# Performance work log

Hardware: AMD Instinct MI355X
Metric: run time of the kernel (lower is better)

The kernel has to match this reference:

```python
import jax, jax.numpy as jnp
import numpy as np

N_NODES = 10000
N_EDGES = 160000
N_GRAPHS = 64
HID = 128
EDGE_DIM = 1
NODE_DIM = 3
LAT = 64
N_LAYERS = 3


def _ln(x, g, b, eps=1e-5):
    m = jnp.mean(x, axis=-1, keepdims=True)
    v = jnp.mean((x - m) ** 2, axis=-1, keepdims=True)
    return (x - m) * jax.lax.rsqrt(v + eps) * g + b


def _lin(x, W, b):
    # torch nn.Linear convention: W is [out, in]
    return x @ W.T + b


def setup_inputs() -> dict:
    key = jax.random.key(0)
    ks = jax.random.split(key, 24)
    s = 0.05
    inp = {
        "x": jax.random.normal(ks[0], (N_NODES, NODE_DIM), jnp.float32),
        "edge_attr": jax.random.normal(ks[1], (N_EDGES, EDGE_DIM), jnp.float32),
        "edge_index": jax.random.randint(ks[2], (2, N_EDGES), 0, N_NODES, jnp.int32),
        "batch": jnp.sort(jax.random.randint(ks[3], (N_NODES,), 0, N_GRAPHS, jnp.int32)),
        # node embedding
        "emb_W": jax.random.normal(ks[4], (HID, NODE_DIM), jnp.float32) * s,
        "emb_b": jnp.zeros((HID,), jnp.float32),
        "emb_ln_g": jnp.ones((HID,), jnp.float32),
        "emb_ln_b": jnp.zeros((HID,), jnp.float32),
        # conv layers (stacked over L)
        "msg1_W": jax.random.normal(ks[5], (N_LAYERS, 2 * HID, 2 * HID + EDGE_DIM), jnp.float32) * s,
        "msg1_b": jnp.zeros((N_LAYERS, 2 * HID), jnp.float32),
        "msg2_W": jax.random.normal(ks[6], (N_LAYERS, HID, 2 * HID), jnp.float32) * s,
        "msg2_b": jnp.zeros((N_LAYERS, HID), jnp.float32),
        "gate_W": jax.random.normal(ks[7], (N_LAYERS, HID, 2 * HID), jnp.float32) * s,
        "gate_b": jnp.zeros((N_LAYERS, HID), jnp.float32),
        "ln_g": jnp.ones((N_LAYERS, HID), jnp.float32),
        "ln_b": jnp.zeros((N_LAYERS, HID), jnp.float32),
        # projector
        "proj1_W": jax.random.normal(ks[8], (HID, HID), jnp.float32) * s,
        "proj1_b": jnp.zeros((HID,), jnp.float32),
        "proj_ln1_g": jnp.ones((HID,), jnp.float32),
        "proj_ln1_b": jnp.zeros((HID,), jnp.float32),
        "proj2_W": jax.random.normal(ks[9], (LAT, HID), jnp.float32) * s,
        "proj2_b": jnp.zeros((LAT,), jnp.float32),
        "proj_ln2_g": jnp.ones((LAT,), jnp.float32),
        "proj_ln2_b": jnp.zeros((LAT,), jnp.float32),
    }
    return inp


def reference(x, edge_attr, edge_index, batch,
              emb_W, emb_b, emb_ln_g, emb_ln_b,
              msg1_W, msg1_b, msg2_W, msg2_b, gate_W, gate_b, ln_g, ln_b,
              proj1_W, proj1_b, proj_ln1_g, proj_ln1_b,
              proj2_W, proj2_b, proj_ln2_g, proj_ln2_b):
    src, dst = edge_index[0], edge_index[1]  # PyG flow source_to_target: x_j=x[src], x_i=x[dst]
    # node embedding
    h = jax.nn.silu(_ln(_lin(x, emb_W, emb_b), emb_ln_g, emb_ln_b))
    for l in range(N_LAYERS):
        z = jnp.concatenate([h[dst], h[src], edge_attr], axis=-1)  # [E, 2H+ed]
        m = jax.nn.silu(_lin(z, msg1_W[l], msg1_b[l]))             # [E, 2H]
        m = _lin(m, msg2_W[l], msg2_b[l])                          # [E, H]
        aggr = jax.ops.segment_sum(m, dst, num_segments=N_NODES)   # scatter-add
        gate = jax.nn.sigmoid(_lin(jnp.concatenate([h, aggr], axis=-1), gate_W[l], gate_b[l]))
        h_new = gate * aggr + (1.0 - gate) * h
        h = _ln(h + h_new, ln_g[l], ln_b[l])
    # global pooling
    counts = jax.ops.segment_sum(jnp.ones((N_NODES,), h.dtype), batch, num_segments=N_GRAPHS)
    sums = jax.ops.segment_sum(h, batch, num_segments=N_GRAPHS)    # [G, H]
    x_mean = sums / jnp.maximum(counts, 1.0)[:, None]
    x_max = sums / (counts[:, None] + 1e-6)
    x_global = x_mean + x_max
    # projector
    p = jax.nn.silu(_ln(_lin(x_global, proj1_W, proj1_b), proj_ln1_g, proj_ln1_b))
    z_out = _ln(_lin(p, proj2_W, proj2_b), proj_ln2_g, proj_ln2_b)
    return z_out, x_global
```

## Files before the change

kernel.cpp:

```cpp
#include <hip/hip_runtime.h>

#define NN 10000
#define NNP 10048
#define NE 160000
#define NG 64
#define HID 128
#define NL 3
#define CAP 64

typedef float floatx4 __attribute__((ext_vector_type(4)));
typedef _Float16 f16x8 __attribute__((ext_vector_type(8)));
typedef __fp16 f16x2 __attribute__((ext_vector_type(2)));

__device__ __forceinline__ float fsig(float x){
  return __builtin_amdgcn_rcpf(1.f + __expf(-x));
}

#define RZ_A (2*65536)
#define RZ_B (RZ_A + NL*32768)
#define RZ_C (RZ_B + NL*32768)
#define RZ_D (RZ_C + NL*256)
#define RB1  1283
#define RB2  (RB1 + 625)
#define RB3  (RB2 + 628)

__global__ __launch_bounds__(256) void k_setup(
    const float* __restrict__ m1, const float* __restrict__ m2,
    const float* __restrict__ mg, const float* __restrict__ m1b,
    const int* __restrict__ ei, const float* __restrict__ ea,
    const float* __restrict__ x,
    const float* __restrict__ eW, const float* __restrict__ eB,
    const float* __restrict__ eG, const float* __restrict__ eBB,
    _Float16* __restrict__ wnf, _Float16* __restrict__ w2f,
    _Float16* __restrict__ gwf, float* __restrict__ w256,
    int* __restrict__ deg, int* __restrict__ esrc2, float* __restrict__ eas2,
    float* __restrict__ hg, _Float16* __restrict__ hfg, _Float16* __restrict__ UV0)
{
  const int bid = blockIdx.x, tid = threadIdx.x;
  if (bid < RB1){
    int i = bid*256 + tid;
    if (i < RZ_A){
      int l = (i>>16) + 1, j = i & 65535;
      int t=j&7, col=(j>>3)&15, quad=(j>>7)&3, s=(j>>9)&3, mb=(j>>11)&31;
      int o = mb*16+col, k = s*32+quad*8+t;
      float v = (o<256) ? m1[l*65792 + o*257 + k] : m1[l*65792 + (o-256)*257 + 128 + k];
      wnf[i] = (_Float16)v;
    } else if (i < RZ_B){
      int j=i-RZ_A; int l=j>>15; j&=32767;
      int t=j&7, col=(j>>3)&15, quad=(j>>7)&3, s=(j>>9)&7, mb=(j>>12)&7;
      w2f[(l<<15)+j] = (_Float16)m2[l*32768 + (mb*16+col)*256 + s*32+quad*8+t];
    } else if (i < RZ_C){
      int j=i-RZ_B; int l=j>>15; j&=32767;
      int t=j&7, col=(j>>3)&15, quad=(j>>7)&3, s=(j>>9)&7, mb=(j>>12)&7;
      gwf[(l<<15)+j] = (_Float16)mg[l*32768 + (mb*16+col)*256 + s*32+quad*8+t];
    } else if (i < RZ_D){
      int j=i-RZ_C; int l=j>>8, o=j&255;
      w256[j] = m1[l*65792 + o*257 + 256];
    }
    return;
  }
  if (bid < RB2){
    int e = (bid-RB1)*256 + tid;
    int d = ei[NE + e];
    int slot = atomicAdd(&deg[d], 1) & (CAP-1);
    esrc2[d*CAP + slot] = ei[e];
    eas2[d*CAP + slot]  = ea[e];
    return;
  }
  __shared__ _Float16 HFs[16][136];
  const int tb = bid - RB2;
  {
    int n = tid>>4, q = tid&15;
    int node = tb*16 + n;
    float x0=0.f, x1=0.f, x2=0.f;
    if (node < NN){ x0=x[node*3]; x1=x[node*3+1]; x2=x[node*3+2]; }
    float v[8], s=0.f, s2=0.f;
#pragma unroll
    for (int j=0;j<8;j++){
      int c = q*8+j;
      v[j] = eW[c*3]*x0 + eW[c*3+1]*x1 + eW[c*3+2]*x2 + eB[c];
      s += v[j]; s2 += v[j]*v[j];
    }
#pragma unroll
    for (int m=1;m<16;m<<=1){ s += __shfl_xor(s,m,64); s2 += __shfl_xor(s2,m,64); }
    float mean = s*(1.f/128.f);
    float var  = s2*(1.f/128.f) - mean*mean;
    float rsq  = rsqrtf(var + 1e-5f);
    float ho[8];
#pragma unroll
    for (int j=0;j<8;j++){
      int c = q*8+j;
      float y = (v[j]-mean)*rsq*eG[c] + eBB[c];
      ho[j] = y * fsig(y);
    }
    *(float4*)(hg + (size_t)node*HID + q*8)     = make_float4(ho[0],ho[1],ho[2],ho[3]);
    *(float4*)(hg + (size_t)node*HID + q*8 + 4) = make_float4(ho[4],ho[5],ho[6],ho[7]);
    union { f16x2 h2[4]; uint4 u; } pk;
    pk.h2[0] = __builtin_amdgcn_cvt_pkrtz(ho[0],ho[1]);
    pk.h2[1] = __builtin_amdgcn_cvt_pkrtz(ho[2],ho[3]);
    pk.h2[2] = __builtin_amdgcn_cvt_pkrtz(ho[4],ho[5]);
    pk.h2[3] = __builtin_amdgcn_cvt_pkrtz(ho[6],ho[7]);
    *(uint4*)(hfg + (size_t)node*HID + q*8) = pk.u;
    *(uint4*)(&HFs[n][q*8]) = pk.u;
  }
  __syncthreads();
  {
    const int wv=tid>>6, lane=tid&63, col=lane&15, quad=lane>>4;
    const int node = tb*16 + col;
    f16x8 bf[4];
#pragma unroll
    for (int s=0;s<4;s++) bf[s] = *(const f16x8*)(&HFs[col][s*32+quad*8]);
#pragma unroll
    for (int mt=0;mt<8;mt++){
      int row = (wv*8+mt)*16 + col;
      const float* wrow = (row<256) ? (m1 + row*257) : (m1 + (row-256)*257 + 128);
      floatx4 acc = (floatx4)(0.f);
#pragma unroll
      for (int s=0;s<4;s++){
        const float* wp = wrow + s*32 + quad*8;
        union { f16x2 h2[4]; f16x8 v8; } pa;
        pa.h2[0] = __builtin_amdgcn_cvt_pkrtz(wp[0],wp[1]);
        pa.h2[1] = __builtin_amdgcn_cvt_pkrtz(wp[2],wp[3]);
        pa.h2[2] = __builtin_amdgcn_cvt_pkrtz(wp[4],wp[5]);
        pa.h2[3] = __builtin_amdgcn_cvt_pkrtz(wp[6],wp[7]);
        acc = __builtin_amdgcn_mfma_f32_16x16x32_f16(pa.v8, bf[s], acc, 0,0,0);
      }
      int o0 = (wv*8+mt)*16 + quad*4;
      float4 bv = (o0 < 256) ? *(const float4*)(m1b + o0) : make_float4(0.f,0.f,0.f,0.f);
      union { f16x2 h2[2]; uint2 u; } pk;
      pk.h2[0] = __builtin_amdgcn_cvt_pkrtz(acc[0]+bv.x, acc[1]+bv.y);
      pk.h2[1] = __builtin_amdgcn_cvt_pkrtz(acc[2]+bv.z, acc[3]+bv.w);
      *(uint2*)(UV0 + (size_t)node*512 + o0) = pk.u;
    }
  }
}

__global__ __launch_bounds__(512) void k_layer(
    const _Float16* __restrict__ uvin, _Float16* __restrict__ uvout,
    const int* __restrict__ esrc2, const float* __restrict__ eas2,
    const int* __restrict__ deg,
    const float* __restrict__ w256l,
    const _Float16* __restrict__ w2fl, const float* __restrict__ b2l,
    const _Float16* __restrict__ gwfl, const float* __restrict__ gbl,
    const float* __restrict__ lngl, const float* __restrict__ lnbl,
    float* __restrict__ hg, _Float16* __restrict__ hfg,
    const _Float16* __restrict__ wnfN, const float* __restrict__ m1bN)
{
  __shared__ _Float16 AggH[16][264];
  __shared__ float    Agg[16][132];
  __shared__ float    reds[8][16], reds2[8][16];
  const int tid = threadIdx.x;
  const int wv = tid>>6, lane = tid&63;
  const int col = lane&15, quad = lane>>4;
  const int half = lane>>5, sub = lane&31;
  const int n0 = blockIdx.x*16;

  {
    const int el = sub*8;
    float wcv[8];
    { float4 a = *(const float4*)(w256l + el);
      float4 b = *(const float4*)(w256l + el + 4);
      wcv[0]=a.x; wcv[1]=a.y; wcv[2]=a.z; wcv[3]=a.w;
      wcv[4]=b.x; wcv[5]=b.y; wcv[6]=b.z; wcv[7]=b.w; }
#pragma unroll
    for (int i=0;i<2;i++){
      int nl = wv*2 + i;
      int n = n0 + nl;
      f16x8 uvec = *(const f16x8*)(uvin + (size_t)n*512 + el);
      float U[8], a[8];
#pragma unroll
      for (int j=0;j<8;j++){ U[j] = (float)uvec[j]; a[j] = 0.f; }
      int dg = deg[n]; if (dg > CAP) dg = CAP;
      int r = half;
      if (r < dg){
        const int*   sp = esrc2 + n*CAP;
        const float* ep = eas2 + n*CAP;
        int src = sp[r]; float eav = ep[r];
        f16x8 vb = *(const f16x8*)(uvin + (size_t)src*512 + 256 + el);
        for (;;){
          int rn = r + 2;
          f16x8 vcur = vb; float eac = eav;
          if (rn < dg){
            int s2 = sp[rn]; eav = ep[rn];
            vb = *(const f16x8*)(uvin + (size_t)s2*512 + 256 + el);
          }
#pragma unroll
          for (int j=0;j<8;j++){
            float f = U[j] + (float)vcur[j] + eac*wcv[j];
            a[j] += f*fsig(f);
          }
          if (rn >= dg) break;
          r = rn;
        }
      }
#pragma unroll
      for (int j=0;j<8;j++) a[j] += __shfl_xor(a[j], 32, 64);
      if (half == 0){
        union { f16x2 h2[4]; uint4 u; } pk;
        pk.h2[0] = __builtin_amdgcn_cvt_pkrtz(a[0],a[1]);
        pk.h2[1] = __builtin_amdgcn_cvt_pkrtz(a[2],a[3]);
        pk.h2[2] = __builtin_amdgcn_cvt_pkrtz(a[4],a[5]);
        pk.h2[3] = __builtin_amdgcn_cvt_pkrtz(a[6],a[7]);
        *(uint4*)(&AggH[nl][el]) = pk.u;
      }
    }
  }
  __syncthreads();

  floatx4 acc2 = (floatx4)(0.f);
  {
    const _Float16* wb2 = w2fl + quad*128 + col*8;
#pragma unroll
    for (int s=0;s<8;s++){
      f16x8 b = *(const f16x8*)(&AggH[col][s*32 + quad*8]);
      f16x8 a = *(const f16x8*)(wb2 + (size_t)(wv*8+s)*512);
      acc2 = __builtin_amdgcn_mfma_f32_16x16x32_f16(a, b, acc2, 0,0,0);
    }
  }
  __syncthreads();
  {
    float degf = (float)deg[n0+col];
    int outb = wv*16 + quad*4;
    float4 b2v = *(const float4*)(b2l + outb);
    float v0 = acc2[0] + degf*b2v.x;
    float v1 = acc2[1] + degf*b2v.y;
    float v2 = acc2[2] + degf*b2v.z;
    float v3 = acc2[3] + degf*b2v.w;
    *(float4*)(&Agg[col][outb]) = make_float4(v0,v1,v2,v3);
    union { f16x2 h2[2]; uint2 u; } pk;
    pk.h2[0] = __builtin_amdgcn_cvt_pkrtz(v0,v1);
    pk.h2[1] = __builtin_amdgcn_cvt_pkrtz(v2,v3);
    *(uint2*)(&AggH[col][outb]) = pk.u;
  }
  __syncthreads();

  floatx4 accg = (floatx4)(0.f);
  {
    const int node = n0 + col;
    const _Float16* wbg = gwfl + quad*128 + col*8;
#pragma unroll
    for (int s=0;s<4;s++){
      f16x8 b = *(const f16x8*)(hfg + (size_t)node*HID + s*32 + quad*8);
      f16x8 a = *(const f16x8*)(wbg + (size_t)(wv*8+s)*512);
      accg = __builtin_amdgcn_mfma_f32_16x16x32_f16(a, b, accg, 0,0,0);
    }
#pragma unroll
    for (int s=4;s<8;s++){
      f16x8 b = *(const f16x8*)(&AggH[col][(s-4)*32 + quad*8]);
      f16x8 a = *(const f16x8*)(wbg + (size_t)(wv*8+s)*512);
      accg = __builtin_amdgcn_mfma_f32_16x16x32_f16(a, b, accg, 0,0,0);
    }
  }
  const int outb = wv*16 + quad*4;
  const int node = n0 + col;
  float vvv[4], ss=0.f, ss2=0.f;
  {
    float4 gbv = *(const float4*)(gbl + outb);
    float4 av  = *(const float4*)(&Agg[col][outb]);
    float4 hv  = *(const float4*)(hg + (size_t)node*HID + outb);
    float gg[4] = {gbv.x,gbv.y,gbv.z,gbv.w};
    float aa[4] = {av.x,av.y,av.z,av.w};
    float hh[4] = {hv.x,hv.y,hv.z,hv.w};
#pragma unroll
    for (int r=0;r<4;r++){
      float gate = fsig(accg[r] + gg[r]);
      float v = hh[r] + gate*aa[r] + (1.f-gate)*hh[r];
      vvv[r] = v; ss += v; ss2 += v*v;
    }
  }
  ss  += __shfl_xor(ss, 16, 64);  ss  += __shfl_xor(ss, 32, 64);
  ss2 += __shfl_xor(ss2, 16, 64); ss2 += __shfl_xor(ss2, 32, 64);
  if (quad == 0){ reds[wv][col] = ss; reds2[wv][col] = ss2; }
  __syncthreads();

  {
    float S=0.f, S2=0.f;
#pragma unroll
    for (int w=0;w<8;w++){ S += reds[w][col]; S2 += reds2[w][col]; }
    float mean = S*(1.f/128.f);
    float var  = S2*(1.f/128.f) - mean*mean;
    float rsq  = rsqrtf(var + 1e-5f);
    float4 gv = *(const float4*)(lngl + outb);
    float4 bv = *(const float4*)(lnbl + outb);
    float o0 = (vvv[0]-mean)*rsq*gv.x + bv.x;
    float o1 = (vvv[1]-mean)*rsq*gv.y + bv.y;
    float o2 = (vvv[2]-mean)*rsq*gv.z + bv.z;
    float o3 = (vvv[3]-mean)*rsq*gv.w + bv.w;
    *(float4*)(hg + (size_t)node*HID + outb) = make_float4(o0,o1,o2,o3);
    union { f16x2 h2[2]; uint2 u; } pk;
    pk.h2[0] = __builtin_amdgcn_cvt_pkrtz(o0,o1);
    pk.h2[1] = __builtin_amdgcn_cvt_pkrtz(o2,o3);
    *(uint2*)(hfg + (size_t)node*HID + outb) = pk.u;
    *(uint2*)(&AggH[col][128 + outb]) = pk.u;
  }
  __syncthreads();

  if (uvout){
    f16x8 bf[4];
#pragma unroll
    for (int s=0;s<4;s++) bf[s] = *(const f16x8*)(&AggH[col][128 + s*32 + quad*8]);
    floatx4 au[4];
#pragma unroll
    for (int i=0;i<4;i++) au[i] = (floatx4)(0.f);
    const _Float16* wbn = wnfN + quad*128 + col*8;
#pragma unroll
    for (int s=0;s<4;s++)
#pragma unroll
      for (int mt=0;mt<4;mt++){
        f16x8 a = *(const f16x8*)(wbn + (size_t)((wv*4+mt)*4+s)*512);
        au[mt] = __builtin_amdgcn_mfma_f32_16x16x32_f16(a, bf[s], au[mt], 0,0,0);
      }
#pragma unroll
    for (int mt=0;mt<4;mt++){
      int o0i = (wv*4+mt)*16 + quad*4;
      float4 buv = (o0i < 256) ? *(const float4*)(m1bN + o0i) : make_float4(0.f,0.f,0.f,0.f);
      union { f16x2 h2[2]; uint2 u; } pu;
      pu.h2[0] = __builtin_amdgcn_cvt_pkrtz(au[mt][0]+buv.x, au[mt][1]+buv.y);
      pu.h2[1] = __builtin_amdgcn_cvt_pkrtz(au[mt][2]+buv.z, au[mt][3]+buv.w);
      *(uint2*)(uvout + (size_t)node*512 + o0i) = pu.u;
    }
  }
}

__global__ __launch_bounds__(512) void k_fin(
    const float* __restrict__ h, const int* __restrict__ batch,
    const float* __restrict__ p1W, const float* __restrict__ p1b,
    const float* __restrict__ l1g, const float* __restrict__ l1b,
    const float* __restrict__ p2W, const float* __restrict__ p2b,
    const float* __restrict__ l2g, const float* __restrict__ l2b,
    float* __restrict__ out)
{
  __shared__ float xs[4][128];
  __shared__ float xg[128], pbuf[128], redf[4];
  const int g = blockIdx.x, tid = threadIdx.x;
  const int c = tid & 127, part = tid >> 7;
  int lo, hi;
  { int L=0, r=NN;
    while (L<r){ int m=(L+r)>>1; if (batch[m]<g) L=m+1; else r=m; }
    lo = L; r = NN;
    while (L<r){ int m=(L+r)>>1; if (batch[m]<g+1) L=m+1; else r=m; }
    hi = L; }
  float s = 0.f;
  for (int n = lo+part; n < hi; n += 4) s += h[(size_t)n*HID + c];
  xs[part][c] = s;
  __syncthreads();
  if (tid < 128){
    float cnt = (float)(hi-lo);
    float S = xs[0][c]+xs[1][c]+xs[2][c]+xs[3][c];
    float xgv = S * (1.f/fmaxf(cnt,1.f) + 1.f/(cnt + 1e-6f));
    out[NG*64 + g*HID + c] = xgv;
    xg[c] = xgv;
  }
  __syncthreads();
  {
    float vp = 0.f;
    for (int k = part*32; k < (part+1)*32; k++) vp += xg[k]*p1W[c*HID + k];
    xs[part][c] = vp;
  }
  __syncthreads();
  float v = 0.f;
  if (tid < 128){
    v = p1b[c] + xs[0][c]+xs[1][c]+xs[2][c]+xs[3][c];
    float sv=v, sv2=v*v;
#pragma unroll
    for (int m=1;m<64;m<<=1){ sv+=__shfl_xor(sv,m,64); sv2+=__shfl_xor(sv2,m,64); }
    if ((c&63)==0){ redf[(c>>6)*2]=sv; redf[(c>>6)*2+1]=sv2; }
  }
  __syncthreads();
  if (tid < 128){
    float S=redf[0]+redf[2], S2=redf[1]+redf[3];
    float mean=S*(1.f/128.f), var=S2*(1.f/128.f)-mean*mean;
    float y=(v-mean)*rsqrtf(var+1e-5f)*l1g[c]+l1b[c];
    pbuf[c] = y*fsig(y);
  }
  __syncthreads();
  if (tid < 64){
    float z = p2b[tid];
    for (int k=0;k<HID;k++) z += pbuf[k]*p2W[tid*HID + k];
    float t=z, t2=z*z;
#pragma unroll
    for (int m=1;m<64;m<<=1){ t+=__shfl_xor(t,m,64); t2+=__shfl_xor(t2,m,64); }
    float mn=t*(1.f/64.f), vr=t2*(1.f/64.f)-mn*mn;
    out[g*64 + tid] = (z-mn)*rsqrtf(vr+1e-5f)*l2g[tid]+l2b[tid];
  }
}

extern "C" void kernel_launch(void* const* d_in, const int* in_sizes, int n_in,
                              void* d_out, int out_size, void* d_ws, size_t ws_size,
                              hipStream_t stream){
  const float* x     = (const float*)d_in[0];
  const float* ea    = (const float*)d_in[1];
  const int*   ei    = (const int*)  d_in[2];
  const int*   batch = (const int*)  d_in[3];
  const float* embW  = (const float*)d_in[4];
  const float* embB  = (const float*)d_in[5];
  const float* embG  = (const float*)d_in[6];
  const float* embBe = (const float*)d_in[7];
  const float* m1W   = (const float*)d_in[8];
  const float* m1b   = (const float*)d_in[9];
  const float* m2W   = (const float*)d_in[10];
  const float* m2b   = (const float*)d_in[11];
  const float* gW    = (const float*)d_in[12];
  const float* gb    = (const float*)d_in[13];
  const float* lng   = (const float*)d_in[14];
  const float* lnb   = (const float*)d_in[15];
  const float* p1W   = (const float*)d_in[16];
  const float* p1b   = (const float*)d_in[17];
  const float* l1g   = (const float*)d_in[18];
  const float* l1b   = (const float*)d_in[19];
  const float* p2W   = (const float*)d_in[20];
  const float* p2b   = (const float*)d_in[21];
  const float* l2g   = (const float*)d_in[22];
  const float* l2b   = (const float*)d_in[23];

  char* p = (char*)d_ws;
  auto alloc = [&](size_t bytes){ char* r = p; p += (bytes + 255) & ~(size_t)255; return r; };
  float*     hg   = (float*)     alloc((size_t)NNP*HID*4);
  _Float16*  hfg  = (_Float16*)  alloc((size_t)NNP*HID*2);
  _Float16*  UVa  = (_Float16*)  alloc((size_t)NNP*512*2);
  _Float16*  UVb  = (_Float16*)  alloc((size_t)NNP*512*2);
  _Float16*  wnf  = (_Float16*)  alloc((size_t)2*65536*2);
  _Float16*  w2f  = (_Float16*)  alloc((size_t)NL*32768*2);
  _Float16*  gwf  = (_Float16*)  alloc((size_t)NL*32768*2);
  float*     w256 = (float*)     alloc((size_t)NL*256*4);
  int*       deg  = (int*)       alloc((size_t)NNP*4);
  int*       esrc2= (int*)       alloc((size_t)NNP*CAP*4);
  float*     eas2 = (float*)     alloc((size_t)NNP*CAP*4);

  hipMemsetAsync(deg, 0, (size_t)NNP*4, stream);

  k_setup<<<RB3, 256, 0, stream>>>(
      m1W, m2W, gW, m1b, ei, ea, x, embW, embB, embG, embBe,
      wnf, w2f, gwf, w256, deg, esrc2, eas2, hg, hfg, UVa);

  for (int l=0; l<NL; l++){
    bool last = (l == NL-1);
    _Float16* uvin  = (l&1) ? UVb : UVa;
    _Float16* uvout = last ? nullptr : ((l&1) ? UVa : UVb);
    k_layer<<<NNP/16, 512, 0, stream>>>(
        uvin, uvout, esrc2, eas2, deg,
        w256 + l*256, w2f + (size_t)l*32768, m2b + l*128,
        gwf + (size_t)l*32768, gb + l*128,
        lng + l*128, lnb + l*128,
        hg, hfg,
        last ? (const _Float16*)nullptr : (wnf + (size_t)l*65536),
        m1b + (last ? 0 : (l+1)*256));
  }
  k_fin<<<NG, 512, 0, stream>>>(hg, batch, p1W, p1b, l1g, l1b,
                                p2W, p2b, l2g, l2b, (float*)d_out);
}
```

Before: 272.8 us.

## Pack edge src/attr into int2 and interleave two-node gather loops

The separate per-slot source-index and edge-attribute arrays are merged into one int2 array, so each edge slot needs a single load. The layer kernel's aggregation now runs the gather loops for its two nodes together, which keeps two independent neighbour loads in flight per iteration to hide gather latency. The embedding part of the setup kernel now processes two 16-node tiles per block, halving that part of the grid. The degree used for the bias term is also clamped to CAP so it matches the number of aggregated edges. Costs are more registers per thread and some idle lanes when the two nodes have different degrees.

```diff
diff --git a/kernel.cpp b/kernel.cpp
--- a/kernel.cpp
+++ b/kernel.cpp
@@ -22,7 +22,7 @@
 #define RZ_D (RZ_C + NL*256)
 #define RB1  1283
 #define RB2  (RB1 + 625)
-#define RB3  (RB2 + 628)
+#define RB3  (RB2 + 314)
 
 __global__ __launch_bounds__(256) void k_setup(
     const float* __restrict__ m1, const float* __restrict__ m2,
@@ -33,7 +33,7 @@
     const float* __restrict__ eG, const float* __restrict__ eBB,
     _Float16* __restrict__ wnf, _Float16* __restrict__ w2f,
     _Float16* __restrict__ gwf, float* __restrict__ w256,
-    int* __restrict__ deg, int* __restrict__ esrc2, float* __restrict__ eas2,
+    int* __restrict__ deg, int2* __restrict__ epk,
     float* __restrict__ hg, _Float16* __restrict__ hfg, _Float16* __restrict__ UV0)
 {
   const int bid = blockIdx.x, tid = threadIdx.x;
@@ -63,82 +63,84 @@
     int e = (bid-RB1)*256 + tid;
     int d = ei[NE + e];
     int slot = atomicAdd(&deg[d], 1) & (CAP-1);
-    esrc2[d*CAP + slot] = ei[e];
-    eas2[d*CAP + slot]  = ea[e];
+    int2 pk; pk.x = ei[e]; pk.y = __float_as_int(ea[e]);
+    epk[(size_t)d*CAP + slot] = pk;
     return;
   }
   __shared__ _Float16 HFs[16][136];
-  const int tb = bid - RB2;
-  {
-    int n = tid>>4, q = tid&15;
-    int node = tb*16 + n;
-    float x0=0.f, x1=0.f, x2=0.f;
-    if (node < NN){ x0=x[node*3]; x1=x[node*3+1]; x2=x[node*3+2]; }
-    float v[8], s=0.f, s2=0.f;
-#pragma unroll
-    for (int j=0;j<8;j++){
-      int c = q*8+j;
-      v[j] = eW[c*3]*x0 + eW[c*3+1]*x1 + eW[c*3+2]*x2 + eB[c];
-      s += v[j]; s2 += v[j]*v[j];
-    }
-#pragma unroll
-    for (int m=1;m<16;m<<=1){ s += __shfl_xor(s,m,64); s2 += __shfl_xor(s2,m,64); }
-    float mean = s*(1.f/128.f);
-    float var  = s2*(1.f/128.f) - mean*mean;
-    float rsq  = rsqrtf(var + 1e-5f);
-    float ho[8];
-#pragma unroll
-    for (int j=0;j<8;j++){
-      int c = q*8+j;
-      float y = (v[j]-mean)*rsq*eG[c] + eBB[c];
-      ho[j] = y * fsig(y);
-    }
-    *(float4*)(hg + (size_t)node*HID + q*8)     = make_float4(ho[0],ho[1],ho[2],ho[3]);
-    *(float4*)(hg + (size_t)node*HID + q*8 + 4) = make_float4(ho[4],ho[5],ho[6],ho[7]);
-    union { f16x2 h2[4]; uint4 u; } pk;
-    pk.h2[0] = __builtin_amdgcn_cvt_pkrtz(ho[0],ho[1]);
-    pk.h2[1] = __builtin_amdgcn_cvt_pkrtz(ho[2],ho[3]);
-    pk.h2[2] = __builtin_amdgcn_cvt_pkrtz(ho[4],ho[5]);
-    pk.h2[3] = __builtin_amdgcn_cvt_pkrtz(ho[6],ho[7]);
-    *(uint4*)(hfg + (size_t)node*HID + q*8) = pk.u;
-    *(uint4*)(&HFs[n][q*8]) = pk.u;
-  }
-  __syncthreads();
-  {
-    const int wv=tid>>6, lane=tid&63, col=lane&15, quad=lane>>4;
-    const int node = tb*16 + col;
-    f16x8 bf[4];
-#pragma unroll
-    for (int s=0;s<4;s++) bf[s] = *(const f16x8*)(&HFs[col][s*32+quad*8]);
-#pragma unroll
-    for (int mt=0;mt<8;mt++){
-      int row = (wv*8+mt)*16 + col;
-      const float* wrow = (row<256) ? (m1 + row*257) : (m1 + (row-256)*257 + 128);
-      floatx4 acc = (floatx4)(0.f);
-#pragma unroll
-      for (int s=0;s<4;s++){
-        const float* wp = wrow + s*32 + quad*8;
-        union { f16x2 h2[4]; f16x8 v8; } pa;
-        pa.h2[0] = __builtin_amdgcn_cvt_pkrtz(wp[0],wp[1]);
-        pa.h2[1] = __builtin_amdgcn_cvt_pkrtz(wp[2],wp[3]);
-        pa.h2[2] = __builtin_amdgcn_cvt_pkrtz(wp[4],wp[5]);
-        pa.h2[3] = __builtin_amdgcn_cvt_pkrtz(wp[6],wp[7]);
-        acc = __builtin_amdgcn_mfma_f32_16x16x32_f16(pa.v8, bf[s], acc, 0,0,0);
-      }
-      int o0 = (wv*8+mt)*16 + quad*4;
-      float4 bv = (o0 < 256) ? *(const float4*)(m1b + o0) : make_float4(0.f,0.f,0.f,0.f);
-      union { f16x2 h2[2]; uint2 u; } pk;
-      pk.h2[0] = __builtin_amdgcn_cvt_pkrtz(acc[0]+bv.x, acc[1]+bv.y);
-      pk.h2[1] = __builtin_amdgcn_cvt_pkrtz(acc[2]+bv.z, acc[3]+bv.w);
-      *(uint2*)(UV0 + (size_t)node*512 + o0) = pk.u;
-    }
+  for (int tt=0; tt<2; tt++){
+    const int tb = (bid - RB2)*2 + tt;
+    {
+      int n = tid>>4, q = tid&15;
+      int node = tb*16 + n;
+      float x0=0.f, x1=0.f, x2=0.f;
+      if (node < NN){ x0=x[node*3]; x1=x[node*3+1]; x2=x[node*3+2]; }
+      float v[8], s=0.f, s2=0.f;
+#pragma unroll
+      for (int j=0;j<8;j++){
+        int c = q*8+j;
+        v[j] = eW[c*3]*x0 + eW[c*3+1]*x1 + eW[c*3+2]*x2 + eB[c];
+        s += v[j]; s2 += v[j]*v[j];
+      }
+#pragma unroll
+      for (int m=1;m<16;m<<=1){ s += __shfl_xor(s,m,64); s2 += __shfl_xor(s2,m,64); }
+      float mean = s*(1.f/128.f);
+      float var  = s2*(1.f/128.f) - mean*mean;
+      float rsq  = rsqrtf(var + 1e-5f);
+      float ho[8];
+#pragma unroll
+      for (int j=0;j<8;j++){
+        int c = q*8+j;
+        float y = (v[j]-mean)*rsq*eG[c] + eBB[c];
+        ho[j] = y * fsig(y);
+      }
+      *(float4*)(hg + (size_t)node*HID + q*8)     = make_float4(ho[0],ho[1],ho[2],ho[3]);
+      *(float4*)(hg + (size_t)node*HID + q*8 + 4) = make_float4(ho[4],ho[5],ho[6],ho[7]);
+      union { f16x2 h2[4]; uint4 u; } pk;
+      pk.h2[0] = __builtin_amdgcn_cvt_pkrtz(ho[0],ho[1]);
+      pk.h2[1] = __builtin_amdgcn_cvt_pkrtz(ho[2],ho[3]);
+      pk.h2[2] = __builtin_amdgcn_cvt_pkrtz(ho[4],ho[5]);
+      pk.h2[3] = __builtin_amdgcn_cvt_pkrtz(ho[6],ho[7]);
+      *(uint4*)(hfg + (size_t)node*HID + q*8) = pk.u;
+      *(uint4*)(&HFs[n][q*8]) = pk.u;
+    }
+    __syncthreads();
+    {
+      const int wv=tid>>6, lane=tid&63, col=lane&15, quad=lane>>4;
+      const int node = tb*16 + col;
+      f16x8 bf[4];
+#pragma unroll
+      for (int s=0;s<4;s++) bf[s] = *(const f16x8*)(&HFs[col][s*32+quad*8]);
+#pragma unroll
+      for (int mt=0;mt<8;mt++){
+        int row = (wv*8+mt)*16 + col;
+        const float* wrow = (row<256) ? (m1 + row*257) : (m1 + (row-256)*257 + 128);
+        floatx4 acc = (floatx4)(0.f);
+#pragma unroll
+        for (int s=0;s<4;s++){
+          const float* wp = wrow + s*32 + quad*8;
+          union { f16x2 h2[4]; f16x8 v8; } pa;
+          pa.h2[0] = __builtin_amdgcn_cvt_pkrtz(wp[0],wp[1]);
+          pa.h2[1] = __builtin_amdgcn_cvt_pkrtz(wp[2],wp[3]);
+          pa.h2[2] = __builtin_amdgcn_cvt_pkrtz(wp[4],wp[5]);
+          pa.h2[3] = __builtin_amdgcn_cvt_pkrtz(wp[6],wp[7]);
+          acc = __builtin_amdgcn_mfma_f32_16x16x32_f16(pa.v8, bf[s], acc, 0,0,0);
+        }
+        int o0 = (wv*8+mt)*16 + quad*4;
+        float4 bv = (o0 < 256) ? *(const float4*)(m1b + o0) : make_float4(0.f,0.f,0.f,0.f);
+        union { f16x2 h2[2]; uint2 u; } pk;
+        pk.h2[0] = __builtin_amdgcn_cvt_pkrtz(acc[0]+bv.x, acc[1]+bv.y);
+        pk.h2[1] = __builtin_amdgcn_cvt_pkrtz(acc[2]+bv.z, acc[3]+bv.w);
+        *(uint2*)(UV0 + (size_t)node*512 + o0) = pk.u;
+      }
+    }
+    __syncthreads();
   }
 }
 
 __global__ __launch_bounds__(512) void k_layer(
     const _Float16* __restrict__ uvin, _Float16* __restrict__ uvout,
-    const int* __restrict__ esrc2, const float* __restrict__ eas2,
-    const int* __restrict__ deg,
+    const int2* __restrict__ epk, const int* __restrict__ deg,
     const float* __restrict__ w256l,
     const _Float16* __restrict__ w2fl, const float* __restrict__ b2l,
     const _Float16* __restrict__ gwfl, const float* __restrict__ gbl,
@@ -162,47 +164,65 @@
       float4 b = *(const float4*)(w256l + el + 4);
       wcv[0]=a.x; wcv[1]=a.y; wcv[2]=a.z; wcv[3]=a.w;
       wcv[4]=b.x; wcv[5]=b.y; wcv[6]=b.z; wcv[7]=b.w; }
-#pragma unroll
-    for (int i=0;i<2;i++){
-      int nl = wv*2 + i;
-      int n = n0 + nl;
-      f16x8 uvec = *(const f16x8*)(uvin + (size_t)n*512 + el);
-      float U[8], a[8];
-#pragma unroll
-      for (int j=0;j<8;j++){ U[j] = (float)uvec[j]; a[j] = 0.f; }
-      int dg = deg[n]; if (dg > CAP) dg = CAP;
-      int r = half;
-      if (r < dg){
-        const int*   sp = esrc2 + n*CAP;
-        const float* ep = eas2 + n*CAP;
-        int src = sp[r]; float eav = ep[r];
-        f16x8 vb = *(const f16x8*)(uvin + (size_t)src*512 + 256 + el);
-        for (;;){
-          int rn = r + 2;
-          f16x8 vcur = vb; float eac = eav;
-          if (rn < dg){
-            int s2 = sp[rn]; eav = ep[rn];
-            vb = *(const f16x8*)(uvin + (size_t)s2*512 + 256 + el);
-          }
-#pragma unroll
-          for (int j=0;j<8;j++){
-            float f = U[j] + (float)vcur[j] + eac*wcv[j];
-            a[j] += f*fsig(f);
-          }
-          if (rn >= dg) break;
-          r = rn;
+
+    const int nA = n0 + wv*2, nB = nA + 1;
+    f16x8 uA = *(const f16x8*)(uvin + (size_t)nA*512 + el);
+    f16x8 uB = *(const f16x8*)(uvin + (size_t)nB*512 + el);
+    float UA[8], UB[8], aA[8], aB[8];
+#pragma unroll
+    for (int j=0;j<8;j++){ UA[j]=(float)uA[j]; UB[j]=(float)uB[j]; aA[j]=0.f; aB[j]=0.f; }
+    int dA = deg[nA]; if (dA > CAP) dA = CAP;
+    int dB = deg[nB]; if (dB > CAP) dB = CAP;
+    const int2* ppA = epk + (size_t)nA*CAP;
+    const int2* ppB = epk + (size_t)nB*CAP;
+
+    f16x8 vA, vB; float eA=0.f, eB=0.f;
+    if (half < dA){ int2 p = ppA[half]; eA = __int_as_float(p.y);
+                    vA = *(const f16x8*)(uvin + (size_t)p.x*512 + 256 + el); }
+    if (half < dB){ int2 p = ppB[half]; eB = __int_as_float(p.y);
+                    vB = *(const f16x8*)(uvin + (size_t)p.x*512 + 256 + el); }
+    int dmax = dA > dB ? dA : dB;
+    for (int r = half; r < dmax; r += 2){
+      bool okA = r < dA, okB = r < dB;
+      f16x8 cA = vA, cB = vB;
+      float ecA = eA, ecB = eB;
+      int rn = r + 2;
+      if (rn < dA){ int2 p = ppA[rn]; eA = __int_as_float(p.y);
+                    vA = *(const f16x8*)(uvin + (size_t)p.x*512 + 256 + el); }
+      if (rn < dB){ int2 p = ppB[rn]; eB = __int_as_float(p.y);
+                    vB = *(const f16x8*)(uvin + (size_t)p.x*512 + 256 + el); }
+      if (okA){
+#pragma unroll
+        for (int j=0;j<8;j++){
+          float f = UA[j] + (float)cA[j] + ecA*wcv[j];
+          aA[j] += f*fsig(f);
         }
       }
-#pragma unroll
-      for (int j=0;j<8;j++) a[j] += __shfl_xor(a[j], 32, 64);
-      if (half == 0){
-        union { f16x2 h2[4]; uint4 u; } pk;
-        pk.h2[0] = __builtin_amdgcn_cvt_pkrtz(a[0],a[1]);
-        pk.h2[1] = __builtin_amdgcn_cvt_pkrtz(a[2],a[3]);
-        pk.h2[2] = __builtin_amdgcn_cvt_pkrtz(a[4],a[5]);
-        pk.h2[3] = __builtin_amdgcn_cvt_pkrtz(a[6],a[7]);
-        *(uint4*)(&AggH[nl][el]) = pk.u;
-      }
+      if (okB){
+#pragma unroll
+        for (int j=0;j<8;j++){
+          float f = UB[j] + (float)cB[j] + ecB*wcv[j];
+          aB[j] += f*fsig(f);
+        }
+      }
+    }
+#pragma unroll
+    for (int j=0;j<8;j++){
+      aA[j] += __shfl_xor(aA[j], 32, 64);
+      aB[j] += __shfl_xor(aB[j], 32, 64);
+    }
+    if (half == 0){
+      union { f16x2 h2[4]; uint4 u; } pk;
+      pk.h2[0] = __builtin_amdgcn_cvt_pkrtz(aA[0],aA[1]);
+      pk.h2[1] = __builtin_amdgcn_cvt_pkrtz(aA[2],aA[3]);
+      pk.h2[2] = __builtin_amdgcn_cvt_pkrtz(aA[4],aA[5]);
+      pk.h2[3] = __builtin_amdgcn_cvt_pkrtz(aA[6],aA[7]);
+      *(uint4*)(&AggH[wv*2][el]) = pk.u;
+      pk.h2[0] = __builtin_amdgcn_cvt_pkrtz(aB[0],aB[1]);
+      pk.h2[1] = __builtin_amdgcn_cvt_pkrtz(aB[2],aB[3]);
+      pk.h2[2] = __builtin_amdgcn_cvt_pkrtz(aB[4],aB[5]);
+      pk.h2[3] = __builtin_amdgcn_cvt_pkrtz(aB[6],aB[7]);
+      *(uint4*)(&AggH[wv*2+1][el]) = pk.u;
     }
   }
   __syncthreads();
@@ -219,7 +239,7 @@
   }
   __syncthreads();
   {
-    float degf = (float)deg[n0+col];
+    float degf = (float)min(deg[n0+col], CAP);
     int outb = wv*16 + quad*4;
     float4 b2v = *(const float4*)(b2l + outb);
     float v0 = acc2[0] + degf*b2v.x;
@@ -424,21 +444,20 @@
   _Float16*  gwf  = (_Float16*)  alloc((size_t)NL*32768*2);
   float*     w256 = (float*)     alloc((size_t)NL*256*4);
   int*       deg  = (int*)       alloc((size_t)NNP*4);
-  int*       esrc2= (int*)       alloc((size_t)NNP*CAP*4);
-  float*     eas2 = (float*)     alloc((size_t)NNP*CAP*4);
+  int2*      epk  = (int2*)      alloc((size_t)NNP*CAP*8);
 
   hipMemsetAsync(deg, 0, (size_t)NNP*4, stream);
 
   k_setup<<<RB3, 256, 0, stream>>>(
       m1W, m2W, gW, m1b, ei, ea, x, embW, embB, embG, embBe,
-      wnf, w2f, gwf, w256, deg, esrc2, eas2, hg, hfg, UVa);
+      wnf, w2f, gwf, w256, deg, epk, hg, hfg, UVa);
 
   for (int l=0; l<NL; l++){
     bool last = (l == NL-1);
     _Float16* uvin  = (l&1) ? UVb : UVa;
     _Float16* uvout = last ? nullptr : ((l&1) ? UVa : UVb);
     k_layer<<<NNP/16, 512, 0, stream>>>(
-        uvin, uvout, esrc2, eas2, deg,
+        uvin, uvout, epk, deg,
         w256 + l*256, w2f + (size_t)l*32768, m2b + l*128,
         gwf + (size_t)l*32768, gb + l*128,
         lng + l*128, lnb + l*128,
```

Measured after the change: 277.5 us. No clear change (+1.7%).

## Split layer-0 node projection into separate MFMA kernel and pack edge src/attr

Applied to the files above, without the earlier changes.

Layer-0 weights are now pre-swizzled to fp16 along with the other layers. The layer-0 node U/V projection moves out of the setup kernel into a new kernel that reads these pre-swizzled weights, instead of converting fp32 weights on the fly with strided loads. Edge source index and edge attribute are packed into one int2 per slot, so the gather loop issues one load instead of two. The degree-times-bias term is now clamped to CAP, and the change adds one more kernel launch.

```diff
diff --git a/kernel.cpp b/kernel.cpp
--- a/kernel.cpp
+++ b/kernel.cpp
@@ -16,31 +16,31 @@
   return __builtin_amdgcn_rcpf(1.f + __expf(-x));
 }
 
-#define RZ_A (2*65536)
+#define RZ_A (NL*65536)
 #define RZ_B (RZ_A + NL*32768)
 #define RZ_C (RZ_B + NL*32768)
 #define RZ_D (RZ_C + NL*256)
-#define RB1  1283
+#define RB1  ((RZ_D + 255)/256)
 #define RB2  (RB1 + 625)
 #define RB3  (RB2 + 628)
 
 __global__ __launch_bounds__(256) void k_setup(
     const float* __restrict__ m1, const float* __restrict__ m2,
-    const float* __restrict__ mg, const float* __restrict__ m1b,
+    const float* __restrict__ mg,
     const int* __restrict__ ei, const float* __restrict__ ea,
     const float* __restrict__ x,
     const float* __restrict__ eW, const float* __restrict__ eB,
     const float* __restrict__ eG, const float* __restrict__ eBB,
     _Float16* __restrict__ wnf, _Float16* __restrict__ w2f,
     _Float16* __restrict__ gwf, float* __restrict__ w256,
-    int* __restrict__ deg, int* __restrict__ esrc2, float* __restrict__ eas2,
-    float* __restrict__ hg, _Float16* __restrict__ hfg, _Float16* __restrict__ UV0)
+    int* __restrict__ deg, int2* __restrict__ epk,
+    float* __restrict__ hg, _Float16* __restrict__ hfg)
 {
   const int bid = blockIdx.x, tid = threadIdx.x;
   if (bid < RB1){
     int i = bid*256 + tid;
     if (i < RZ_A){
-      int l = (i>>16) + 1, j = i & 65535;
+      int l = i>>16, j = i & 65535;
       int t=j&7, col=(j>>3)&15, quad=(j>>7)&3, s=(j>>9)&3, mb=(j>>11)&31;
       int o = mb*16+col, k = s*32+quad*8+t;
       float v = (o<256) ? m1[l*65792 + o*257 + k] : m1[l*65792 + (o-256)*257 + 128 + k];
@@ -63,82 +63,86 @@
     int e = (bid-RB1)*256 + tid;
     int d = ei[NE + e];
     int slot = atomicAdd(&deg[d], 1) & (CAP-1);
-    esrc2[d*CAP + slot] = ei[e];
-    eas2[d*CAP + slot]  = ea[e];
+    int2 pk; pk.x = ei[e]; pk.y = __float_as_int(ea[e]);
+    epk[(size_t)d*CAP + slot] = pk;
     return;
   }
-  __shared__ _Float16 HFs[16][136];
   const int tb = bid - RB2;
-  {
-    int n = tid>>4, q = tid&15;
-    int node = tb*16 + n;
-    float x0=0.f, x1=0.f, x2=0.f;
-    if (node < NN){ x0=x[node*3]; x1=x[node*3+1]; x2=x[node*3+2]; }
-    float v[8], s=0.f, s2=0.f;
-#pragma unroll
-    for (int j=0;j<8;j++){
-      int c = q*8+j;
-      v[j] = eW[c*3]*x0 + eW[c*3+1]*x1 + eW[c*3+2]*x2 + eB[c];
-      s += v[j]; s2 += v[j]*v[j];
-    }
-#pragma unroll
-    for (int m=1;m<16;m<<=1){ s += __shfl_xor(s,m,64); s2 += __shfl_xor(s2,m,64); }
-    float mean = s*(1.f/128.f);
-    float var  = s2*(1.f/128.f) - mean*mean;
-    float rsq  = rsqrtf(var + 1e-5f);
-    float ho[8];
-#pragma unroll
-    for (int j=0;j<8;j++){
-      int c = q*8+j;
-      float y = (v[j]-mean)*rsq*eG[c] + eBB[c];
-      ho[j] = y * fsig(y);
-    }
-    *(float4*)(hg + (size_t)node*HID + q*8)     = make_float4(ho[0],ho[1],ho[2],ho[3]);
-    *(float4*)(hg + (size_t)node*HID + q*8 + 4) = make_float4(ho[4],ho[5],ho[6],ho[7]);
-    union { f16x2 h2[4]; uint4 u; } pk;
-    pk.h2[0] = __builtin_amdgcn_cvt_pkrtz(ho[0],ho[1]);
-    pk.h2[1] = __builtin_amdgcn_cvt_pkrtz(ho[2],ho[3]);
-    pk.h2[2] = __builtin_amdgcn_cvt_pkrtz(ho[4],ho[5]);
-    pk.h2[3] = __builtin_amdgcn_cvt_pkrtz(ho[6],ho[7]);
-    *(uint4*)(hfg + (size_t)node*HID + q*8) = pk.u;
-    *(uint4*)(&HFs[n][q*8]) = pk.u;
-  }
-  __syncthreads();
-  {
-    const int wv=tid>>6, lane=tid&63, col=lane&15, quad=lane>>4;
-    const int node = tb*16 + col;
-    f16x8 bf[4];
-#pragma unroll
-    for (int s=0;s<4;s++) bf[s] = *(const f16x8*)(&HFs[col][s*32+quad*8]);
+  int n = tid>>4, q = tid&15;
+  int node = tb*16 + n;
+  float x0=0.f, x1=0.f, x2=0.f;
+  if (node < NN){ x0=x[node*3]; x1=x[node*3+1]; x2=x[node*3+2]; }
+  float v[8], s=0.f, s2=0.f;
+#pragma unroll
+  for (int j=0;j<8;j++){
+    int c = q*8+j;
+    v[j] = eW[c*3]*x0 + eW[c*3+1]*x1 + eW[c*3+2]*x2 + eB[c];
+    s += v[j]; s2 += v[j]*v[j];
+  }
+#pragma unroll
+  for (int m=1;m<16;m<<=1){ s += __shfl_xor(s,m,64); s2 += __shfl_xor(s2,m,64); }
+  float mean = s*(1.f/128.f);
+  float var  = s2*(1.f/128.f) - mean*mean;
+  float rsq  = rsqrtf(var + 1e-5f);
+  float ho[8];
+#pragma unroll
+  for (int j=0;j<8;j++){
+    int c = q*8+j;
+    float y = (v[j]-mean)*rsq*eG[c] + eBB[c];
+    ho[j] = y * fsig(y);
+  }
+  *(float4*)(hg + (size_t)node*HID + q*8)     = make_float4(ho[0],ho[1],ho[2],ho[3]);
+  *(float4*)(hg + (size_t)node*HID + q*8 + 4) = make_float4(ho[4],ho[5],ho[6],ho[7]);
+  union { f16x2 h2[4]; uint4 u; } pk;
+  pk.h2[0] = __builtin_amdgcn_cvt_pkrtz(ho[0],ho[1]);
+  pk.h2[1] = __builtin_amdgcn_cvt_pkrtz(ho[2],ho[3]);
+  pk.h2[2] = __builtin_amdgcn_cvt_pkrtz(ho[4],ho[5]);
+  pk.h2[3] = __builtin_amdgcn_cvt_pkrtz(ho[6],ho[7]);
+  *(uint4*)(hfg + (size_t)node*HID + q*8) = pk.u;
+}
+
+__global__ __launch_bounds__(256) void k_nodeUV(
+    const _Float16* __restrict__ hf,
+    const _Float16* __restrict__ wnf, const float* __restrict__ m1b,
+    _Float16* __restrict__ UV)
+{
+  const int tid = threadIdx.x;
+  const int wv = tid>>6, lane = tid&63;
+  const int col = lane&15, quad = lane>>4;
+  const int node = blockIdx.x*16 + col;
+
+  f16x8 bfrag[4];
+#pragma unroll
+  for (int s=0;s<4;s++)
+    bfrag[s] = *(const f16x8*)(hf + (size_t)node*HID + s*32 + quad*8);
+
+  floatx4 acc[8];
+#pragma unroll
+  for (int i=0;i<8;i++) acc[i] = (floatx4)(0.f);
+
+  const _Float16* wb = wnf + quad*128 + col*8;
+#pragma unroll
+  for (int s=0;s<4;s++)
 #pragma unroll
     for (int mt=0;mt<8;mt++){
-      int row = (wv*8+mt)*16 + col;
-      const float* wrow = (row<256) ? (m1 + row*257) : (m1 + (row-256)*257 + 128);
-      floatx4 acc = (floatx4)(0.f);
-#pragma unroll
-      for (int s=0;s<4;s++){
-        const float* wp = wrow + s*32 + quad*8;
-        union { f16x2 h2[4]; f16x8 v8; } pa;
-        pa.h2[0] = __builtin_amdgcn_cvt_pkrtz(wp[0],wp[1]);
-        pa.h2[1] = __builtin_amdgcn_cvt_pkrtz(wp[2],wp[3]);
-        pa.h2[2] = __builtin_amdgcn_cvt_pkrtz(wp[4],wp[5]);
-        pa.h2[3] = __builtin_amdgcn_cvt_pkrtz(wp[6],wp[7]);
-        acc = __builtin_amdgcn_mfma_f32_16x16x32_f16(pa.v8, bf[s], acc, 0,0,0);
-      }
-      int o0 = (wv*8+mt)*16 + quad*4;
-      float4 bv = (o0 < 256) ? *(const float4*)(m1b + o0) : make_float4(0.f,0.f,0.f,0.f);
-      union { f16x2 h2[2]; uint2 u; } pk;
-      pk.h2[0] = __builtin_amdgcn_cvt_pkrtz(acc[0]+bv.x, acc[1]+bv.y);
-      pk.h2[1] = __builtin_amdgcn_cvt_pkrtz(acc[2]+bv.z, acc[3]+bv.w);
-      *(uint2*)(UV0 + (size_t)node*512 + o0) = pk.u;
-    }
+      f16x8 a = *(const f16x8*)(wb + (size_t)((wv*8+mt)*4+s)*512);
+      acc[mt] = __builtin_amdgcn_mfma_f32_16x16x32_f16(a, bfrag[s], acc[mt], 0,0,0);
+    }
+
+#pragma unroll
+  for (int mt=0;mt<8;mt++){
+    int o0 = wv*128 + mt*16 + quad*4;
+    float4 bv = (o0 < 256) ? *(const float4*)(m1b + o0) : make_float4(0.f,0.f,0.f,0.f);
+    union { f16x2 h2[2]; uint2 u; } pk;
+    pk.h2[0] = __builtin_amdgcn_cvt_pkrtz(acc[mt][0]+bv.x, acc[mt][1]+bv.y);
+    pk.h2[1] = __builtin_amdgcn_cvt_pkrtz(acc[mt][2]+bv.z, acc[mt][3]+bv.w);
+    *(uint2*)(UV + (size_t)node*512 + o0) = pk.u;
   }
 }
 
 __global__ __launch_bounds__(512) void k_layer(
     const _Float16* __restrict__ uvin, _Float16* __restrict__ uvout,
-    const int* __restrict__ esrc2, const float* __restrict__ eas2,
-    const int* __restrict__ deg,
+    const int2* __restrict__ epk, const int* __restrict__ deg,
     const float* __restrict__ w256l,
     const _Float16* __restrict__ w2fl, const float* __restrict__ b2l,
     const _Float16* __restrict__ gwfl, const float* __restrict__ gbl,
@@ -171,18 +175,19 @@
 #pragma unroll
       for (int j=0;j<8;j++){ U[j] = (float)uvec[j]; a[j] = 0.f; }
       int dg = deg[n]; if (dg > CAP) dg = CAP;
+      const int2* pp = epk + (size_t)n*CAP;
       int r = half;
       if (r < dg){
-        const int*   sp = esrc2 + n*CAP;
-        const float* ep = eas2 + n*CAP;
-        int src = sp[r]; float eav = ep[r];
-        f16x8 vb = *(const f16x8*)(uvin + (size_t)src*512 + 256 + el);
+        int2 p0 = pp[r];
+        float eav = __int_as_float(p0.y);
+        f16x8 vb = *(const f16x8*)(uvin + (size_t)p0.x*512 + 256 + el);
         for (;;){
           int rn = r + 2;
           f16x8 vcur = vb; float eac = eav;
           if (rn < dg){
-            int s2 = sp[rn]; eav = ep[rn];
-            vb = *(const f16x8*)(uvin + (size_t)s2*512 + 256 + el);
+            int2 p = pp[rn];
+            eav = __int_as_float(p.y);
+            vb = *(const f16x8*)(uvin + (size_t)p.x*512 + 256 + el);
           }
 #pragma unroll
           for (int j=0;j<8;j++){
@@ -219,7 +224,7 @@
   }
   __syncthreads();
   {
-    float degf = (float)deg[n0+col];
+    float degf = (float)min(deg[n0+col], CAP);
     int outb = wv*16 + quad*4;
     float4 b2v = *(const float4*)(b2l + outb);
     float v0 = acc2[0] + degf*b2v.x;
@@ -419,31 +424,32 @@
   _Float16*  hfg  = (_Float16*)  alloc((size_t)NNP*HID*2);
   _Float16*  UVa  = (_Float16*)  alloc((size_t)NNP*512*2);
   _Float16*  UVb  = (_Float16*)  alloc((size_t)NNP*512*2);
-  _Float16*  wnf  = (_Float16*)  alloc((size_t)2*65536*2);
+  _Float16*  wnf  = (_Float16*)  alloc((size_t)NL*65536*2);
   _Float16*  w2f  = (_Float16*)  alloc((size_t)NL*32768*2);
   _Float16*  gwf  = (_Float16*)  alloc((size_t)NL*32768*2);
   float*     w256 = (float*)     alloc((size_t)NL*256*4);
   int*       deg  = (int*)       alloc((size_t)NNP*4);
-  int*       esrc2= (int*)       alloc((size_t)NNP*CAP*4);
-  float*     eas2 = (float*)     alloc((size_t)NNP*CAP*4);
+  int2*      epk  = (int2*)      alloc((size_t)NNP*CAP*8);
 
   hipMemsetAsync(deg, 0, (size_t)NNP*4, stream);
 
   k_setup<<<RB3, 256, 0, stream>>>(
-      m1W, m2W, gW, m1b, ei, ea, x, embW, embB, embG, embBe,
-      wnf, w2f, gwf, w256, deg, esrc2, eas2, hg, hfg, UVa);
+      m1W, m2W, gW, ei, ea, x, embW, embB, embG, embBe,
+      wnf, w2f, gwf, w256, deg, epk, hg, hfg);
+
+  k_nodeUV<<<NNP/16, 256, 0, stream>>>(hfg, wnf, m1b, UVa);
 
   for (int l=0; l<NL; l++){
     bool last = (l == NL-1);
     _Float16* uvin  = (l&1) ? UVb : UVa;
     _Float16* uvout = last ? nullptr : ((l&1) ? UVa : UVb);
     k_layer<<<NNP/16, 512, 0, stream>>>(
-        uvin, uvout, esrc2, eas2, deg,
+        uvin, uvout, epk, deg,
         w256 + l*256, w2f + (size_t)l*32768, m2b + l*128,
         gwf + (size_t)l*32768, gb + l*128,
         lng + l*128, lnb + l*128,
         hg, hfg,
-        last ? (const _Float16*)nullptr : (wnf + (size_t)l*65536),
+        last ? (const _Float16*)nullptr : (wnf + (size_t)(l+1)*65536),
         m1b + (last ? 0 : (l+1)*256));
   }
   k_fin<<<NG, 512, 0, stream>>>(hg, batch, p1W, p1b, l1g, l1b,
```

New measurement: 251.6 us. 7.8% less time.
